# Performance work log

Hardware: AMD Instinct MI355X
Metric: run time of the kernel (lower is better)

The kernel has to match this reference:

```python
import math
import jax, jax.numpy as jnp
import numpy as np

V, S, D, H, HID, L, B = 32000, 1024, 768, 12, 3072, 4, 2
HD = D // H
EPS = 1e-5
CLAMP = 1e9


def setup_inputs() -> dict:
    key = jax.random.key(0)
    ks = jax.random.split(key, 10)
    std = 0.02
    return {
        "W_emb": jax.random.normal(ks[0], (V, D), jnp.float32) * std,      # tied with lm_head
        "pos_emb": jax.random.normal(ks[1], (S, D), jnp.float32) * std,
        "norm1_g": jnp.ones((L, D), jnp.float32),
        "norm1_b": jnp.zeros((L, D), jnp.float32),
        "qkv_w": jax.random.normal(ks[2], (L, 3 * D, D), jnp.float32) * std,
        "qkv_b": jnp.zeros((L, 3 * D), jnp.float32),
        "proj_w": jax.random.normal(ks[3], (L, D, D), jnp.float32) * std,
        "proj_b": jnp.zeros((L, D), jnp.float32),
        "norm2_g": jnp.ones((L, D), jnp.float32),
        "norm2_b": jnp.zeros((L, D), jnp.float32),
        "ffn_w1": jax.random.normal(ks[4], (L, HID, D), jnp.float32) * std,
        "ffn_b1": jnp.zeros((L, HID), jnp.float32),
        "ffn_w2": jax.random.normal(ks[5], (L, D, HID), jnp.float32) * std,
        "ffn_b2": jnp.zeros((L, D), jnp.float32),
        "fin_g": jnp.ones((D,), jnp.float32),
        "fin_b": jnp.zeros((D,), jnp.float32),
        "input_ids": jax.random.randint(ks[6], (B, S), 0, V, jnp.int64),
    }


def layer_norm(x, g, b):
    mean = jnp.mean(x, axis=-1, keepdims=True)
    var = jnp.mean((x - mean) ** 2, axis=-1, keepdims=True)
    return g * ((x - mean) / jnp.sqrt(var + EPS)) + b


def attention(x, qkv_w, qkv_b, proj_w, proj_b):
    b, s, _ = x.shape
    qkv = x @ qkv_w.T + qkv_b                                  # [B,S,3D]
    qkv = qkv.reshape(b, s, H, 3 * HD).transpose(0, 2, 1, 3)   # [B,H,S,3*HD]
    q, k, v = qkv[..., :HD], qkv[..., HD:2 * HD], qkv[..., 2 * HD:]
    scaled = jnp.einsum("bhqd,bhkd->bhqk", q, k) / math.sqrt(HD)
    mask = jnp.tril(jnp.ones((s, s), bool))
    scaled = jnp.clip(jnp.where(mask, scaled, -jnp.inf), -CLAMP, CLAMP)
    attn = jax.nn.softmax(scaled, axis=-1)
    vals = jnp.einsum("bhqk,bhkd->bhqd", attn, v)
    vals = vals.transpose(0, 2, 1, 3).reshape(b, s, D)
    return vals @ proj_w.T + proj_b


def reference(W_emb, pos_emb, norm1_g, norm1_b, qkv_w, qkv_b, proj_w, proj_b,
              norm2_g, norm2_b, ffn_w1, ffn_b1, ffn_w2, ffn_b2, fin_g, fin_b,
              input_ids):
    x = W_emb[input_ids] * math.sqrt(D)          # [B,S,D]
    x = x + pos_emb[None, :x.shape[1], :]
    for i in range(L):
        h = layer_norm(x, norm1_g[i], norm1_b[i])
        x = x + attention(h, qkv_w[i], qkv_b[i], proj_w[i], proj_b[i])
        h = layer_norm(x, norm2_g[i], norm2_b[i])
        h = jax.nn.gelu(h @ ffn_w1[i].T + ffn_b1[i], approximate=False)
        x = x + h @ ffn_w2[i].T + ffn_b2[i]
    x = layer_norm(x, fin_g, fin_b)
    logits = x @ W_emb.T                         # tied lm_head, no bias
    return logits
```

## Files before the change

kernel.cpp:

```cpp
#include <hip/hip_runtime.h>
#include <hip/hip_bf16.h>
#include <math.h>

typedef __bf16 bf16_t;
typedef __bf16 bf16x8 __attribute__((ext_vector_type(8)));
typedef float f32x4 __attribute__((ext_vector_type(4)));

__device__ __forceinline__ void gload16(const bf16_t* g, bf16_t* l) {
  __builtin_amdgcn_global_load_lds(
      (const __attribute__((address_space(1))) unsigned int*)g,
      (__attribute__((address_space(3))) unsigned int*)l, 16, 0, 0);
}


template<int EPI>
__global__ __launch_bounds__(128, 3) void gemm_bt(
    const bf16_t* __restrict__ A, const bf16_t* __restrict__ W,
    const float* __restrict__ bias,
    bf16_t* __restrict__ obf, float* __restrict__ of32, bf16_t* __restrict__ vt,
    int M, int N, int K, int kLen)
{
  __shared__ bf16_t As[128 * 64];
  __shared__ bf16_t Bs[64 * 64];
  const int tid  = threadIdx.x;
  const int lane = tid & 63;
  const int w    = tid >> 6;
  const long m0 = (long)blockIdx.y * 128;
  const long n0 = (long)blockIdx.x * 64;
  const int k0 = blockIdx.z * kLen;
  const int k1 = k0 + kLen;

  f32x4 acc[4][4] = {};

  const int l7  = lane & 7;
  const int l15 = lane & 15;
  const int hi  = lane >> 4;
  const int rA  = w * 64 + l15;

  for (int kt = k0; kt < k1; kt += 64) {
#pragma unroll
    for (int i = 0; i < 8; ++i) {
      const int cl  = tid + i * 128;
      const int row = cl >> 3;
      const int j   = (cl & 7) ^ (row & 7);
      gload16(A + (m0 + row) * K + kt + (j << 3), As + cl * 8);
    }
#pragma unroll
    for (int i = 0; i < 4; ++i) {
      const int cl  = tid + i * 128;
      const int row = cl >> 3;
      const int j   = (cl & 7) ^ (row & 7);
      gload16(W + (n0 + row) * K + kt + (j << 3), Bs + cl * 8);
    }
    __syncthreads();
#pragma unroll
    for (int kk = 0; kk < 64; kk += 32) {
      const int ck = ((((kk >> 3) + hi) ^ l7) << 3);
      bf16x8 af[4], bfr[4];
#pragma unroll
      for (int m = 0; m < 4; ++m) af[m]  = *(const bf16x8*)(As + (rA + m * 16) * 64 + ck);
#pragma unroll
      for (int n = 0; n < 4; ++n) bfr[n] = *(const bf16x8*)(Bs + (l15 + n * 16) * 64 + ck);
#pragma unroll
      for (int m = 0; m < 4; ++m)
#pragma unroll
        for (int n = 0; n < 4; ++n)
          acc[m][n] = __builtin_amdgcn_mfma_f32_16x16x32_bf16(af[m], bfr[n], acc[m][n], 0, 0, 0);
    }
    __syncthreads();
  }

  const int lr = hi << 2;
#pragma unroll
  for (int n = 0; n < 4; ++n) {
    const long gcol = n0 + n * 16 + l15;
    float bv = 0.f;
    if (EPI == 0 || EPI == 1 || EPI == 5) bv = bias[gcol];
    if (EPI == 6 && k0 == 0)  bv = bias[gcol];
    const int hq = (int)gcol / 192;
    const int c  = (int)gcol - hq * 192;
#pragma unroll
    for (int m = 0; m < 4; ++m) {
      const long grow0 = m0 + w * 64 + m * 16 + lr;
#pragma unroll
      for (int r = 0; r < 4; ++r) {
        float v = acc[m][n][r] + bv;
        const long idx = (grow0 + r) * N + gcol;
        if (EPI == 0 || EPI == 5) {
          obf[idx] = (bf16_t)v;
          if (EPI == 5 && c >= 128) {
            const int row = (int)(grow0 + r);
            const int bb = row >> 10, ss = row & 1023;
            vt[(((long)bb * 12 + hq) * 64 + (c - 128)) * 1024 + ss] = (bf16_t)v;
          }
        } else if (EPI == 1) {
          v = 0.5f * v * (1.0f + erff(v * 0.70710678118654752f));
          obf[idx] = (bf16_t)v;
        } else {
          of32[(long)blockIdx.z * ((long)M * N) + idx] = v;
        }
      }
    }
  }
}

__global__ __launch_bounds__(256, 3) void gemm_logits(
    const bf16_t* __restrict__ A, const bf16_t* __restrict__ W,
    float* __restrict__ out)
{
  __shared__ bf16_t As[128 * 64];
  __shared__ bf16_t Bs[128 * 64];
  const int tid  = threadIdx.x;
  const int lane = tid & 63;
  const int w    = tid >> 6;
  const int wr   = w >> 1;
  const int wc   = w & 1;
  const int d    = blockIdx.x;
  const int wk   = (d & 7) * 500 + (d >> 3);
  const long m0  = (long)(wk & 15) * 128;
  const long n0  = (long)(wk >> 4) * 128;
  const int K = 768, N = 32000;

  f32x4 acc[4][4] = {};
  const int l7  = lane & 7;
  const int l15 = lane & 15;
  const int hi  = lane >> 4;
  const int rA  = wr * 64 + l15;
  const int rB  = wc * 64 + l15;

  for (int kt = 0; kt < K; kt += 64) {
#pragma unroll
    for (int i = 0; i < 4; ++i) {
      const int cl  = tid + i * 256;
      const int row = cl >> 3;
      const int j   = (cl & 7) ^ (row & 7);
      gload16(A + (m0 + row) * K + kt + (j << 3), As + cl * 8);
    }
#pragma unroll
    for (int i = 0; i < 4; ++i) {
      const int cl  = tid + i * 256;
      const int row = cl >> 3;
      const int j   = (cl & 7) ^ (row & 7);
      gload16(W + (n0 + row) * K + kt + (j << 3), Bs + cl * 8);
    }
    __syncthreads();
#pragma unroll
    for (int kk = 0; kk < 64; kk += 32) {
      const int ck = ((((kk >> 3) + hi) ^ l7) << 3);
      bf16x8 af[4], bfr[4];
#pragma unroll
      for (int m = 0; m < 4; ++m) af[m]  = *(const bf16x8*)(As + (rA + m * 16) * 64 + ck);
#pragma unroll
      for (int n = 0; n < 4; ++n) bfr[n] = *(const bf16x8*)(Bs + (rB + n * 16) * 64 + ck);
#pragma unroll
      for (int m = 0; m < 4; ++m)
#pragma unroll
        for (int n = 0; n < 4; ++n)
          acc[m][n] = __builtin_amdgcn_mfma_f32_16x16x32_bf16(af[m], bfr[n], acc[m][n], 0, 0, 0);
    }
    __syncthreads();
  }

  const int lr = hi << 2;
#pragma unroll
  for (int n = 0; n < 4; ++n) {
    const long gcol = n0 + wc * 64 + n * 16 + l15;
#pragma unroll
    for (int m = 0; m < 4; ++m) {
      const long grow0 = m0 + wr * 64 + m * 16 + lr;
#pragma unroll
      for (int r = 0; r < 4; ++r)
        __builtin_nontemporal_store(acc[m][n][r], &out[(grow0 + r) * N + gcol]);
    }
  }
}

__global__ __launch_bounds__(256) void attn_kernel(
    const bf16_t* __restrict__ qkv, const bf16_t* __restrict__ vT,
    bf16_t* __restrict__ aout)
{
  __shared__ bf16_t Plds[4][16 * 64];
  const int tid  = threadIdx.x;
  const int lane = tid & 63;
  const int w    = tid >> 6;
  const int bh   = blockIdx.x >> 4;
  const int k    = blockIdx.x & 15;
  const int qt   = (w < 2) ? (2 * k + w) : (63 - 2 * k - (w & 1));
  const int b    = bh / 12;
  const int h    = bh % 12;
  const int q0   = qt << 4;

  const bf16_t* base = qkv + (long)b * 1024 * 2304 + h * 192;
  const bf16_t* vtb  = vT + (long)bh * 64 * 1024;
  const int koff  = (lane >> 4) << 3;
  const int l15   = lane & 15;
  const int rbase = (lane >> 4) << 2;

  const bf16x8 qf0 = *(const bf16x8*)(base + (long)(q0 + l15) * 2304 + koff);
  const bf16x8 qf1 = *(const bf16x8*)(base + (long)(q0 + l15) * 2304 + 32 + koff);

  f32x4 acc[4] = {};
  float mrun[4], lrun[4];
#pragma unroll
  for (int r = 0; r < 4; ++r) { mrun[r] = -1e30f; lrun[r] = 0.f; }

  bf16_t* pl = &Plds[w][0];
  const int kbmax = (q0 + 15) >> 6;
  for (int kb = 0; kb <= kbmax; ++kb) {
    const int kv0 = kb << 6;
    const f32x4 z = {0.f, 0.f, 0.f, 0.f};
    f32x4 s[4];
    __builtin_amdgcn_s_setprio(1);
#pragma unroll
    for (int g = 0; g < 4; ++g) {
      const bf16_t* kr = base + 64 + (long)(kv0 + g * 16 + l15) * 2304;
      const bf16x8 ka = *(const bf16x8*)(kr + koff);
      const bf16x8 kb2 = *(const bf16x8*)(kr + 32 + koff);
      s[g] = __builtin_amdgcn_mfma_f32_16x16x32_bf16(qf0, ka, z, 0, 0, 0);
      s[g] = __builtin_amdgcn_mfma_f32_16x16x32_bf16(qf1, kb2, s[g], 0, 0, 0);
    }
    __builtin_amdgcn_s_setprio(0);

#pragma unroll
    for (int r = 0; r < 4; ++r) {
      const int qi = q0 + rbase + r;
      float v[4];
#pragma unroll
      for (int g = 0; g < 4; ++g)
        v[g] = (kv0 + g * 16 + l15 <= qi) ? s[g][r] * 0.125f : -1e9f;
      float mx = fmaxf(fmaxf(v[0], v[1]), fmaxf(v[2], v[3]));
#pragma unroll
      for (int dd = 1; dd < 16; dd <<= 1) mx = fmaxf(mx, __shfl_xor(mx, dd));
      if (mx > mrun[r] + 8.f) {
        const float sc = __expf(mrun[r] - mx);
        lrun[r] *= sc;
        acc[0][r] *= sc; acc[1][r] *= sc; acc[2][r] *= sc; acc[3][r] *= sc;
        mrun[r] = mx;
      }
      float p[4], sm = 0.f;
#pragma unroll
      for (int g = 0; g < 4; ++g) { p[g] = __expf(v[g] - mrun[r]); sm += p[g]; }
#pragma unroll
      for (int dd = 1; dd < 16; dd <<= 1) sm += __shfl_xor(sm, dd);
      lrun[r] += sm;
#pragma unroll
      for (int g = 0; g < 4; ++g)
        pl[(rbase + r) * 64 + g * 16 + l15] = (bf16_t)p[g];
    }
    asm volatile("s_waitcnt lgkmcnt(0)" ::: "memory");
    const bf16x8 pf0 = *(const bf16x8*)(pl + l15 * 64 + koff);
    const bf16x8 pf1 = *(const bf16x8*)(pl + l15 * 64 + 32 + koff);
    __builtin_amdgcn_s_setprio(1);
#pragma unroll
    for (int hh = 0; hh < 2; ++hh) {
      const bf16x8 pf = hh ? pf1 : pf0;
      const int sbase = kv0 + hh * 32 + koff;
#pragma unroll
      for (int cb = 0; cb < 4; ++cb) {
        const bf16x8 vf = *(const bf16x8*)(vtb + (long)(cb * 16 + l15) * 1024 + sbase);
        acc[cb] = __builtin_amdgcn_mfma_f32_16x16x32_bf16(pf, vf, acc[cb], 0, 0, 0);
      }
    }
    __builtin_amdgcn_s_setprio(0);
  }

#pragma unroll
  for (int cb = 0; cb < 4; ++cb)
#pragma unroll
    for (int r = 0; r < 4; ++r) {
      const float o = acc[cb][r] / lrun[r];
      aout[(long)(b * 1024 + q0 + rbase + r) * 768 + h * 64 + cb * 16 + l15] = (bf16_t)o;
    }
}

__global__ __launch_bounds__(256) void ln_fuse2(
    float* __restrict__ x, const float* __restrict__ dl,
    const float* __restrict__ g, const float* __restrict__ bta,
    bf16_t* __restrict__ out)
{
  const int row = blockIdx.x;
  const int tid = threadIdx.x;
  float* xr = x + (long)row * 768;
  const float* d0 = dl + (long)row * 768;
  const float* d1 = d0 + 1572864;
  float v[3];
#pragma unroll
  for (int k = 0; k < 3; ++k) {
    const int c = tid + k * 256;
    const float t = xr[c] + d0[c] + d1[c];
    v[k] = t;
    xr[c] = t;
  }
  float s  = v[0] + v[1] + v[2];
  float ss = v[0] * v[0] + v[1] * v[1] + v[2] * v[2];
#pragma unroll
  for (int d = 1; d < 64; d <<= 1) { s += __shfl_xor(s, d); ss += __shfl_xor(ss, d); }
  __shared__ float sh[8];
  const int lane = tid & 63, wv = tid >> 6;
  if (lane == 0) { sh[wv] = s; sh[4 + wv] = ss; }
  __syncthreads();
  s  = sh[0] + sh[1] + sh[2] + sh[3];
  ss = sh[4] + sh[5] + sh[6] + sh[7];
  const float mean = s * (1.0f / 768.0f);
  const float var  = ss * (1.0f / 768.0f) - mean * mean;
  const float inv  = rsqrtf(var + 1e-5f);
  bf16_t* orow = out + (long)row * 768;
#pragma unroll
  for (int k = 0; k < 3; ++k) {
    const int c = tid + k * 256;
    orow[c] = (bf16_t)(g[c] * ((v[k] - mean) * inv) + bta[c]);
  }
}

__global__ __launch_bounds__(256) void embed_ln(
    const int* __restrict__ ids, const float* __restrict__ We,
    const float* __restrict__ pos, const float* __restrict__ g,
    const float* __restrict__ bta, float* __restrict__ x,
    bf16_t* __restrict__ out)
{
  const int row = blockIdx.x;
  const int tid = threadIdx.x;
  const int sidx = row & 1023;
  const long id = ids[row];
  const float* wr = We + id * 768;
  const float* pr = pos + (long)sidx * 768;
  float* xr = x + (long)row * 768;
  float v[3];
#pragma unroll
  for (int k = 0; k < 3; ++k) {
    const int c = tid + k * 256;
    const float t = wr[c] * 27.712812921102035f + pr[c];
    v[k] = t;
    xr[c] = t;
  }
  float s  = v[0] + v[1] + v[2];
  float ss = v[0] * v[0] + v[1] * v[1] + v[2] * v[2];
#pragma unroll
  for (int d = 1; d < 64; d <<= 1) { s += __shfl_xor(s, d); ss += __shfl_xor(ss, d); }
  __shared__ float sh[8];
  const int lane = tid & 63, wv = tid >> 6;
  if (lane == 0) { sh[wv] = s; sh[4 + wv] = ss; }
  __syncthreads();
  s  = sh[0] + sh[1] + sh[2] + sh[3];
  ss = sh[4] + sh[5] + sh[6] + sh[7];
  const float mean = s * (1.0f / 768.0f);
  const float var  = ss * (1.0f / 768.0f) - mean * mean;
  const float inv  = rsqrtf(var + 1e-5f);
  bf16_t* orow = out + (long)row * 768;
#pragma unroll
  for (int k = 0; k < 3; ++k) {
    const int c = tid + k * 256;
    orow[c] = (bf16_t)(g[c] * ((v[k] - mean) * inv) + bta[c]);
  }
}

__global__ __launch_bounds__(256) void cvt_all_kernel(
    const float* __restrict__ s0, const float* __restrict__ s1,
    const float* __restrict__ s2, const float* __restrict__ s3,
    const float* __restrict__ s4, bf16_t* __restrict__ out)
{
  const int b = blockIdx.x;
  const float* src; long rel, obase;
  if      (b < 3456)  { src = s0; rel = (long)b * 2048;          obase = 0;        }
  else if (b < 4608)  { src = s1; rel = (long)(b - 3456) * 2048; obase = 7077888;  }
  else if (b < 9216)  { src = s2; rel = (long)(b - 4608) * 2048; obase = 9437184;  }
  else if (b < 13824) { src = s3; rel = (long)(b - 9216) * 2048; obase = 18874368; }
  else                { src = s4; rel = (long)(b - 13824) * 2048; obase = 28311552; }
  const long i = rel + (long)threadIdx.x * 8;
  const f32x4 a = *(const f32x4*)(src + i);
  const f32x4 c = *(const f32x4*)(src + i + 4);
  bf16x8 o;
#pragma unroll
  for (int j = 0; j < 4; ++j) { o[j] = (bf16_t)a[j]; o[4 + j] = (bf16_t)c[j]; }
  *(bf16x8*)(out + obase + i) = o;
}

extern "C" void kernel_launch(void* const* d_in, const int* in_sizes, int n_in,
                              void* d_out, int out_size, void* d_ws, size_t ws_size,
                              hipStream_t stream)
{
  const float* W_emb = (const float*)d_in[0];
  const float* pos   = (const float*)d_in[1];
  const float* n1g   = (const float*)d_in[2];
  const float* n1b   = (const float*)d_in[3];
  const float* qkvw  = (const float*)d_in[4];
  const float* qkvb  = (const float*)d_in[5];
  const float* projw = (const float*)d_in[6];
  const float* projb = (const float*)d_in[7];
  const float* n2g   = (const float*)d_in[8];
  const float* n2b   = (const float*)d_in[9];
  const float* f1w   = (const float*)d_in[10];
  const float* f1b   = (const float*)d_in[11];
  const float* f2w   = (const float*)d_in[12];
  const float* f2b   = (const float*)d_in[13];
  const float* fing  = (const float*)d_in[14];
  const float* finb  = (const float*)d_in[15];
  const int*   ids   = (const int*)d_in[16];
  float* out = (float*)d_out;

  char* ws = (char*)d_ws;
  float*  x     = (float*)(ws);
  bf16_t* h     = (bf16_t*)(ws + 6291456);
  bf16_t* qkv   = (bf16_t*)(ws + 9437184);
  bf16_t* attn  = (bf16_t*)(ws + 18874368);
  bf16_t* ffn1o = (bf16_t*)(ws + 22020096);
  bf16_t* Wq    = (bf16_t*)(ws + 34603008);
  bf16_t* Wp    = (bf16_t*)(ws + 48758784);
  bf16_t* W1    = (bf16_t*)(ws + 53477376);
  bf16_t* W2    = (bf16_t*)(ws + 72351744);
  bf16_t* We    = (bf16_t*)(ws + 91226112);
  bf16_t* vT    = (bf16_t*)(ws + 140378112);
  float*  dpart = (float*)(ws + 143523840);

  cvt_all_kernel<<<dim3(25824), 256, 0, stream>>>(qkvw, projw, f1w, f2w, W_emb, Wq);

  embed_ln<<<2048, 256, 0, stream>>>(ids, W_emb, pos, n1g, n1b, x, h);

  for (int i = 0; i < 4; ++i) {
    if (i > 0)
      ln_fuse2<<<2048, 256, 0, stream>>>(x, dpart, n1g + i * 768, n1b + i * 768, h);
    gemm_bt<5><<<dim3(36, 16), 128, 0, stream>>>(
        h, Wq + (long)i * 2304 * 768, qkvb + i * 2304, qkv, nullptr, vT,
        2048, 2304, 768, 768);
    attn_kernel<<<384, 256, 0, stream>>>(qkv, vT, attn);
    gemm_bt<6><<<dim3(12, 16, 2), 128, 0, stream>>>(
        attn, Wp + (long)i * 768 * 768, projb + i * 768, nullptr, dpart, nullptr,
        2048, 768, 768, 384);
    ln_fuse2<<<2048, 256, 0, stream>>>(x, dpart, n2g + i * 768, n2b + i * 768, h);
    gemm_bt<1><<<dim3(48, 16), 128, 0, stream>>>(
        h, W1 + (long)i * 3072 * 768, f1b + i * 3072, ffn1o, nullptr, nullptr,
        2048, 3072, 768, 768);
    gemm_bt<6><<<dim3(12, 16, 2), 128, 0, stream>>>(
        ffn1o, W2 + (long)i * 768 * 3072, f2b + i * 768, nullptr, dpart, nullptr,
        2048, 768, 3072, 1536);
  }
  ln_fuse2<<<2048, 256, 0, stream>>>(x, dpart, fing, finb, h);
  gemm_logits<<<dim3(4000), 256, 0, stream>>>(h, We, out);
}
```

Baseline: 767.9 us.

## Use 128x128 four-wave GEMM tiles for QKV and FFN1 projections

Adds a gemm_bt2 kernel with 256 threads and a 128x128 output tile (2x2 waves of 64x64), and uses it for the QKV and FFN1 GEMMs in place of the 128x64 two-wave kernel. The larger N tile raises operand reuse per LDS load and halves the number of blocks, aiming to cut global and LDS traffic per FLOP. The old kernel is reduced to the split-K fp32 epilogue path. The trade-off is fewer blocks (288 and 384), so CU occupancy may be lower on a 256-CU device.

```diff
diff --git a/kernel.cpp b/kernel.cpp
--- a/kernel.cpp
+++ b/kernel.cpp
@@ -75,29 +75,101 @@
   for (int n = 0; n < 4; ++n) {
     const long gcol = n0 + n * 16 + l15;
     float bv = 0.f;
-    if (EPI == 0 || EPI == 1 || EPI == 5) bv = bias[gcol];
     if (EPI == 6 && k0 == 0)  bv = bias[gcol];
-    const int hq = (int)gcol / 192;
-    const int c  = (int)gcol - hq * 192;
 #pragma unroll
     for (int m = 0; m < 4; ++m) {
       const long grow0 = m0 + w * 64 + m * 16 + lr;
+#pragma unroll
+      for (int r = 0; r < 4; ++r) {
+        const float v = acc[m][n][r] + bv;
+        const long idx = (grow0 + r) * N + gcol;
+        of32[(long)blockIdx.z * ((long)M * N) + idx] = v;
+      }
+    }
+  }
+}
+
+template<int EPI>
+__global__ __launch_bounds__(256, 3) void gemm_bt2(
+    const bf16_t* __restrict__ A, const bf16_t* __restrict__ W,
+    const float* __restrict__ bias,
+    bf16_t* __restrict__ obf, bf16_t* __restrict__ vt,
+    int M, int N, int K)
+{
+  __shared__ bf16_t As[128 * 64];
+  __shared__ bf16_t Bs[128 * 64];
+  const int tid  = threadIdx.x;
+  const int lane = tid & 63;
+  const int w    = tid >> 6;
+  const int wr   = w >> 1;
+  const int wc   = w & 1;
+  const long m0 = (long)blockIdx.y * 128;
+  const long n0 = (long)blockIdx.x * 128;
+
+  f32x4 acc[4][4] = {};
+  const int l7  = lane & 7;
+  const int l15 = lane & 15;
+  const int hi  = lane >> 4;
+  const int rA  = wr * 64 + l15;
+  const int rB  = wc * 64 + l15;
+
+  for (int kt = 0; kt < K; kt += 64) {
+#pragma unroll
+    for (int i = 0; i < 4; ++i) {
+      const int cl  = tid + i * 256;
+      const int row = cl >> 3;
+      const int j   = (cl & 7) ^ (row & 7);
+      gload16(A + (m0 + row) * K + kt + (j << 3), As + cl * 8);
+    }
+#pragma unroll
+    for (int i = 0; i < 4; ++i) {
+      const int cl  = tid + i * 256;
+      const int row = cl >> 3;
+      const int j   = (cl & 7) ^ (row & 7);
+      gload16(W + (n0 + row) * K + kt + (j << 3), Bs + cl * 8);
+    }
+    __syncthreads();
+#pragma unroll
+    for (int kk = 0; kk < 64; kk += 32) {
+      const int ck = ((((kk >> 3) + hi) ^ l7) << 3);
+      bf16x8 af[4], bfr[4];
+#pragma unroll
+      for (int m = 0; m < 4; ++m) af[m]  = *(const bf16x8*)(As + (rA + m * 16) * 64 + ck);
+#pragma unroll
+      for (int n = 0; n < 4; ++n) bfr[n] = *(const bf16x8*)(Bs + (rB + n * 16) * 64 + ck);
+#pragma unroll
+      for (int m = 0; m < 4; ++m)
+#pragma unroll
+        for (int n = 0; n < 4; ++n)
+          acc[m][n] = __builtin_amdgcn_mfma_f32_16x16x32_bf16(af[m], bfr[n], acc[m][n], 0, 0, 0);
+    }
+    __syncthreads();
+  }
+
+  const int lr = hi << 2;
+#pragma unroll
+  for (int n = 0; n < 4; ++n) {
+    const long gcol = n0 + wc * 64 + n * 16 + l15;
+    const float bv = bias[gcol];
+    int hq = 0, c = 0;
+    if (EPI == 5) { hq = (int)gcol / 192; c = (int)gcol - hq * 192; }
+#pragma unroll
+    for (int m = 0; m < 4; ++m) {
+      const long grow0 = m0 + wr * 64 + m * 16 + lr;
 #pragma unroll
       for (int r = 0; r < 4; ++r) {
         float v = acc[m][n][r] + bv;
         const long idx = (grow0 + r) * N + gcol;
-        if (EPI == 0 || EPI == 5) {
+        if (EPI == 5) {
           obf[idx] = (bf16_t)v;
-          if (EPI == 5 && c >= 128) {
+          if (c >= 128) {
             const int row = (int)(grow0 + r);
             const int bb = row >> 10, ss = row & 1023;
             vt[(((long)bb * 12 + hq) * 64 + (c - 128)) * 1024 + ss] = (bf16_t)v;
           }
-        } else if (EPI == 1) {
+        } else {
           v = 0.5f * v * (1.0f + erff(v * 0.70710678118654752f));
           obf[idx] = (bf16_t)v;
-        } else {
-          of32[(long)blockIdx.z * ((long)M * N) + idx] = v;
         }
       }
     }
@@ -419,17 +491,15 @@
   for (int i = 0; i < 4; ++i) {
     if (i > 0)
       ln_fuse2<<<2048, 256, 0, stream>>>(x, dpart, n1g + i * 768, n1b + i * 768, h);
-    gemm_bt<5><<<dim3(36, 16), 128, 0, stream>>>(
-        h, Wq + (long)i * 2304 * 768, qkvb + i * 2304, qkv, nullptr, vT,
-        2048, 2304, 768, 768);
+    gemm_bt2<5><<<dim3(18, 16), 256, 0, stream>>>(
+        h, Wq + (long)i * 2304 * 768, qkvb + i * 2304, qkv, vT, 2048, 2304, 768);
     attn_kernel<<<384, 256, 0, stream>>>(qkv, vT, attn);
     gemm_bt<6><<<dim3(12, 16, 2), 128, 0, stream>>>(
         attn, Wp + (long)i * 768 * 768, projb + i * 768, nullptr, dpart, nullptr,
         2048, 768, 768, 384);
     ln_fuse2<<<2048, 256, 0, stream>>>(x, dpart, n2g + i * 768, n2b + i * 768, h);
-    gemm_bt<1><<<dim3(48, 16), 128, 0, stream>>>(
-        h, W1 + (long)i * 3072 * 768, f1b + i * 3072, ffn1o, nullptr, nullptr,
-        2048, 3072, 768, 768);
+    gemm_bt2<1><<<dim3(24, 16), 256, 0, stream>>>(
+        h, W1 + (long)i * 3072 * 768, f1b + i * 3072, ffn1o, nullptr, 2048, 3072, 768);
     gemm_bt<6><<<dim3(12, 16, 2), 128, 0, stream>>>(
         ffn1o, W2 + (long)i * 768 * 3072, f2b + i * 768, nullptr, dpart, nullptr,
         2048, 768, 3072, 1536);
```

Measured after the change: 789.0 us. 1.03x slower.
